# Performance work log

Hardware: AMD Instinct MI355X
Metric: run time of the kernel (lower is better)

Reference implementation:

```python
import math
import jax, jax.numpy as jnp
import numpy as np

N_ORDERS = 2
CHUNK = 64  # tokens per chunk (before virtual-token expansion)


def _expand_derivative(x, n):
    """expand_virtual_tokens(mode='derivative'): [B,H,S,D] -> [B,H,S*n,D]."""
    B, H, S, D = x.shape
    pad = jnp.zeros((B, H, n - 1, D), x.dtype)
    xp = jnp.concatenate([pad, x], axis=2)  # [B,H,S+n-1,D]
    coeffs = np.array([(-1) ** kk * math.comb(n - 1, kk) for kk in range(n)], dtype=np.float32)
    coeffs = coeffs / np.abs(coeffs).sum()  # L1-normalized binomial coeffs
    # window j at token t is x_pad[t+j]*coeffs[j]; then flip window dim (as in torch .flip(-1))
    win = jnp.stack([xp[:, :, j:j + S, :] * coeffs[j] for j in range(n)], axis=3)  # [B,H,S,n,D]
    win = win[:, :, :, ::-1, :]
    return win.reshape(B, H, S * n, D)


def _unlinear(x, scale=2.0):
    """unlinear_activation: gated norm-scaled gelu applied to inter-chunk state."""
    xn = jnp.linalg.norm(x, axis=-1, keepdims=True) + 1e-6
    return x / scale * jax.nn.gelu(scale * x / xn, approximate=True)


def _stab(x):
    # ensure_stability: clamp to [-1e4, 1e4], nan -> center (0)
    return jnp.nan_to_num(jnp.clip(x, -1e4, 1e4), nan=0.0, posinf=1e4, neginf=-1e4)


def _forward(q, k, v, beta):
    n = N_ORDERS
    B, H, S, D = q.shape
    qe = _expand_derivative(q, n)
    ke = _expand_derivative(k, n)
    ve = _expand_derivative(v, n)
    be = jnp.repeat(beta, n, axis=-1)[..., None]  # [B,H,S*n,1]
    w = ke * be  # delta-rule write keys
    u = ve * be  # delta-rule write values

    Cn = CHUNK * n                     # virtual tokens per chunk
    NC = (S * n) // Cn                 # number of chunks
    ch = lambda x: x.reshape(B, H, NC, Cn, D)
    qc, kc, wc, uc = ch(qe), ch(ke), ch(w), ch(u)

    # triangular (forward-substitution) inversion per chunk:
    # T = (I + tril(W K^T, -1))^{-1}  == fast_invert_matrix of the strictly-lower system
    A = jnp.tril(jnp.einsum('bhnid,bhnjd->bhnij', wc, kc), -1)
    eye = jnp.eye(Cn, dtype=q.dtype)
    T = jax.scipy.linalg.solve_triangular(
        eye + A, jnp.broadcast_to(eye, A.shape), lower=True, unit_diagonal=True)
    wci = jnp.einsum('bhnij,bhnjd->bhnid', T, wc)
    uci = jnp.einsum('bhnij,bhnjd->bhnid', T, uc)

    def chunk_step(h, xs):
        # sequential_delta_product_scan body: per-token Householder updates, n_orders steps
        qx, wx, ux = xs  # each [B,H,Cn,D]
        C = CHUNK
        qr = qx.reshape(B, H, C, n, D)
        wr = wx.reshape(B, H, C, n, D)
        ur = ux.reshape(B, H, C, n, D)
        state = jnp.broadcast_to(h[:, :, None], (B, H, C, D, D))  # per-token state
        outs = []
        for s in range(n):
            qs, ws, us = qr[:, :, :, s], wr[:, :, :, s], ur[:, :, :, s]
            kho = jnp.einsum('bhcd,bhcde->bhce', ws, state)
            uval = us - kho
            o_inter = jnp.einsum('bhcd,bhcde->bhce', qs, state)
            o_intra = qs * uval
            state = _stab(state + jnp.einsum('bhcd,bhce->bhcde', ws, uval))
            outs.append(o_intra + o_inter)
        o = jnp.stack(outs, axis=3).reshape(B, H, C * n, D)  # interleave: pos t*n+s
        h_new = _unlinear(state[:, :, -1])  # linear_activation=False path
        return h_new, o

    xs = (jnp.moveaxis(qc, 2, 0), jnp.moveaxis(wci, 2, 0), jnp.moveaxis(uci, 2, 0))
    h0 = jnp.zeros((B, H, D, D), q.dtype)
    _, os = jax.lax.scan(chunk_step, h0, xs)  # os: [NC,B,H,Cn,D]
    out_v = jnp.moveaxis(os, 0, 2).reshape(B, H, S, n, D)
    return out_v[..., n - 1, :]  # collapse virtual tokens: keep last-order output per token


def setup_inputs() -> dict:
    key = jax.random.key(0)
    kq, kk, kv, kb = jax.random.split(key, 4)
    B, H, S, D = 2, 16, 2048, 64
    return {
        'q': jax.random.normal(kq, (B, H, S, D), jnp.float32),
        'k': jax.random.normal(kk, (B, H, S, D), jnp.float32),
        'v': jax.random.normal(kv, (B, H, S, D), jnp.float32),
        'beta': jax.random.uniform(kb, (B, H, S), jnp.float32),
    }


def reference(q, k, v, beta):
    return _forward(q, k, v, beta)
```

## Files before the change

### kernel.cpp

```cpp
#include <hip/hip_runtime.h>
#include <math.h>


namespace {
constexpr int PAIRS = 32;
constexpr int SLEN  = 2048;
constexpr int D     = 64;
constexpr int CK    = 64;
constexpr int CN    = 128;
constexpr int NCH   = 32;
constexpr int NB2   = 16;
constexpr int NP    = 5;
constexpr size_t YWORDS = (size_t)PAIRS * NCH * CN * CN;
constexpr int GP = 2145;
constexpr size_t GGW = (size_t)PAIRS * NCH * GP;
constexpr size_t HGW = (size_t)PAIRS * (NCH + 1) * D * D;

__device__ __forceinline__ float stab1(float x) {
    float y = __builtin_amdgcn_fmed3f(x, -10000.f, 10000.f);
    return (x != x) ? 0.f : y;
}

__device__ __forceinline__ int kidx(int a, int f4) {
    return a * 68 + 4 * (f4 ^ ((a >> 2) & 3));
}
}

__global__ __launch_bounds__(256, 2)
void la_gram(const float* __restrict__ kg, float* __restrict__ gG)
{
    __shared__ float kstf[65 * 68];
    const int blk = blockIdx.x;
    const int p = blk >> 5, nc = blk & 31;
    const int tid = threadIdx.x;
    const int baseT = nc * CK;
    const float* kp = kg + (size_t)p * SLEN * D;

    for (int u = tid; u < 65 * 16; u += 256) {
        int a = u >> 4, f4 = u & 15;
        int src = baseT - 1 + a;
        float4 val = float4{0.f, 0.f, 0.f, 0.f};
        if (src >= 0) val = ((const float4*)(kp + (size_t)src * D))[f4];
        *(float4*)&kstf[kidx(a, f4)] = val;
    }
    __syncthreads();

    float* gps = gG + (size_t)blk * GP;
    for (int tt = tid; tt < 17 * 17; tt += 256) {
        int ta = tt / 17, tb = tt % 17;
        if (tb > ta) continue;
        int a0 = ta * 4, b0 = tb * 4;
        float acc[4][4] = {};
        for (int d4 = 0; d4 < 16; ++d4) {
            float4 av[4], bv[4];
            #pragma unroll
            for (int r = 0; r < 4; ++r) {
                av[r] = *(const float4*)&kstf[kidx(min(a0 + r, 64), d4)];
                bv[r] = *(const float4*)&kstf[kidx(min(b0 + r, 64), d4)];
            }
            #pragma unroll
            for (int r = 0; r < 4; ++r)
                #pragma unroll
                for (int c = 0; c < 4; ++c)
                    acc[r][c] += av[r].x * bv[c].x + av[r].y * bv[c].y
                               + av[r].z * bv[c].z + av[r].w * bv[c].w;
        }
        #pragma unroll
        for (int r = 0; r < 4; ++r)
            #pragma unroll
            for (int c = 0; c < 4; ++c) {
                int a = a0 + r, b = b0 + c;
                if (a <= 64 && b <= a)
                    gps[a * (a + 1) / 2 + b] = acc[r][c];
            }
    }
}

__global__ __launch_bounds__(256, 3)
void la_phase1g(const float* __restrict__ kg, const float* __restrict__ vg,
                const float* __restrict__ bg, float* __restrict__ ws,
                const float* __restrict__ gG)
{
    __shared__ float Ysh[CN][64];
    __shared__ float scm[2][CN][8];
    __shared__ float redsh[24][66];
    __shared__ float bq4[CK], bh[CK];

    const int blk  = blockIdx.x;
    const int p    = blk >> 6;
    const int nc   = (blk >> 1) & 31;
    const int half = blk & 1;
    const int tid  = threadIdx.x;
    const int col  = tid & 63;
    const int m    = tid >> 6;
    const int baseT = nc * CK;
    const float* kp = kg + (size_t)p * SLEN * D;
    const float* vp = vg + (size_t)p * SLEN * D;
    const float* bp = bg + (size_t)p * SLEN;
    const float* gps = gG + (size_t)(p * NCH + nc) * GP;

    if (tid < CK) {
        float bv = bp[baseT + tid];
        bq4[tid] = 0.25f * bv;
        bh[tid]  = 0.5f  * bv;
    }
    __syncthreads();

    const float* srcBase = half ? vp : kp;
    for (int u = tid; u < CN * 16; u += 256) {
        int i = u >> 4, f4 = u & 15;
        int ci = i >> 1, si = i & 1;
        float sc = si ? bh[ci] : -bh[ci];
        int srcT = baseT + ci - si;
        float4 val = float4{0.f, 0.f, 0.f, 0.f};
        if (srcT >= 0) val = ((const float4*)(srcBase + (size_t)srcT * D))[f4];
        val.x *= sc; val.y *= sc; val.z *= sc; val.w *= sc;
        *(float4*)&Ysh[i][f4 * 4] = val;
    }
    for (int e = tid; e < 64; e += 256) {
        int j = e >> 3, r = e & 7;
        int ai = (r >> 1) - (r & 1) + 1;
        int aj = (j >> 1) - (j & 1) + 1;
        int amax = max(ai, aj), amin = min(ai, aj);
        float sgn = ((r ^ j) & 1) ? -1.f : 1.f;
        scm[0][j][r] = sgn * bq4[r >> 1] * gps[amax * (amax + 1) / 2 + amin];
    }
    __syncthreads();

    for (int g = 0; g < 16; ++g) {
        const int buf = g & 1;
        float acc[8] = {};
        for (int j = m; j < 8 * g; j += 4) {
            float yv = Ysh[j][col];
            const float4 a03 = *(const float4*)&scm[buf][j][0];
            const float4 a47 = *(const float4*)&scm[buf][j][4];
            acc[0] += a03.x * yv; acc[1] += a03.y * yv;
            acc[2] += a03.z * yv; acc[3] += a03.w * yv;
            acc[4] += a47.x * yv; acc[5] += a47.y * yv;
            acc[6] += a47.z * yv; acc[7] += a47.w * yv;
        }
        if (m > 0) {
            #pragma unroll
            for (int r = 0; r < 8; ++r) redsh[(m - 1) * 8 + r][col] = acc[r];
        }
        __syncthreads();
        if (m == 0) {
            if (g > 0) {
                #pragma unroll
                for (int r = 0; r < 8; ++r)
                    acc[r] += redsh[r][col] + redsh[8 + r][col] + redsh[16 + r][col];
            }
            float yn[8];
            #pragma unroll
            for (int r = 0; r < 8; ++r) {
                float val = Ysh[8 * g + r][col] - acc[r];
                #pragma unroll
                for (int rp = 0; rp < 8; ++rp)
                    if (rp < r) val -= scm[buf][8 * g + rp][r] * yn[rp];
                yn[r] = val;
                Ysh[8 * g + r][col] = val;
            }
        } else if (g < 15) {
            const int T = g + 1, bufB = T & 1;
            const int nel = 8 * (8 * T + 8);
            for (int e = tid - 64; e < nel; e += 192) {
                int j = e >> 3, r = e & 7;
                int i = 8 * T + r;
                int ai = (i >> 1) - (i & 1) + 1;
                int aj = (j >> 1) - (j & 1) + 1;
                int amax = max(ai, aj), amin = min(ai, aj);
                float sgn = ((i ^ j) & 1) ? -1.f : 1.f;
                scm[bufB][j][r] = sgn * bq4[i >> 1] * gps[amax * (amax + 1) / 2 + amin];
            }
        }
        __syncthreads();
    }

    float* gY = ws + (size_t)(p * NCH + nc) * (CN * CN) + half * 64;
    for (int u = tid; u < CN * 16; u += 256) {
        int r = u >> 4, f4 = u & 15;
        *(float4*)&gY[r * CN + f4 * 4] = *(const float4*)&Ysh[r][f4 * 4];
    }
}

__global__ __launch_bounds__(512, 1)
void la_scan(const float* __restrict__ ws, float* __restrict__ hg)
{
    __shared__ float w0s[64], u0s[64], w1s[64], u1s[64];
    __shared__ float pA[8][64], pB[8][64];
    __shared__ float hsh2[64][67];

    const int p = blockIdx.x;
    const int tid = threadIdx.x;
    const int w = tid >> 6, lane = tid & 63;
    const int hd = tid >> 3, he0 = (tid & 7) * 8;
    const float* Yp = ws + (size_t)p * NCH * (CN * CN);
    float* hp = hg + (size_t)p * (NCH + 1) * (D * D);

    for (int idx = tid; idx < D * D; idx += 512) hp[idx] = 0.f;
    for (int idx = tid; idx < 64 * 67; idx += 512) (&hsh2[0][0])[idx] = 0.f;

    auto stagew = [&](float v) {
        if (tid < 64)       w0s[tid] = v;
        else if (tid < 128) u0s[tid - 64] = v;
        else if (tid < 192) w1s[tid - 128] = v;
        else if (tid < 256) u1s[tid - 192] = v;
    };
    {
        float v = 0.f;
        if (tid < 256) v = Yp[(size_t)(126 + (tid >> 7)) * CN + (tid & 127)];
        stagew(v);
    }
    float hs[8];
    #pragma unroll
    for (int j = 0; j < 8; ++j) hs[j] = 0.f;
    __syncthreads();

    for (int nc = 0; nc < NCH; ++nc) {
        float pf = 0.f;
        if (nc + 1 < NCH && tid < 256)
            pf = Yp[(size_t)(nc + 1) * (CN * CN)
                    + (size_t)(126 + (tid >> 7)) * CN + (tid & 127)];

        float s = 0.f;
        #pragma unroll
        for (int j = 0; j < 8; ++j) s += w0s[8 * w + j] * hs[j];
        pA[w][lane] = s;
        __syncthreads();

        float sum = 0.f;
        #pragma unroll
        for (int wv = 0; wv < 8; ++wv) sum += pA[wv][lane];
        const float uv0 = u0s[lane] - sum;

        float st1[8];
        float s2 = 0.f;
        #pragma unroll
        for (int j = 0; j < 8; ++j) {
            st1[j] = stab1(hs[j] + w0s[8 * w + j] * uv0);
            s2 += w1s[8 * w + j] * st1[j];
        }
        pB[w][lane] = s2;
        __syncthreads();

        float sum2 = 0.f;
        #pragma unroll
        for (int wv = 0; wv < 8; ++wv) sum2 += pB[wv][lane];
        const float uv1 = u1s[lane] - sum2;
        #pragma unroll
        for (int j = 0; j < 8; ++j)
            hsh2[8 * w + j][lane] = stab1(st1[j] + w1s[8 * w + j] * uv1);
        __syncthreads();

        {
            float st2v[8];
            float ssum = 0.f;
            #pragma unroll
            for (int j = 0; j < 8; ++j) {
                st2v[j] = hsh2[hd][he0 + j];
                ssum += st2v[j] * st2v[j];
            }
            ssum += __shfl_xor(ssum, 1);
            ssum += __shfl_xor(ssum, 2);
            ssum += __shfl_xor(ssum, 4);
            float xn = __builtin_amdgcn_sqrtf(ssum) + 1e-6f;
            float sc2 = 2.f * __builtin_amdgcn_rcpf(xn);
            float hn[8];
            #pragma unroll
            for (int j = 0; j < 8; ++j) {
                float x  = st2v[j];
                float y  = x * sc2;
                float y2 = y * y;
                float e  = __builtin_amdgcn_exp2f(y * (2.3022078f + 0.1029432f * y2));
                float th = (e - 1.f) * __builtin_amdgcn_rcpf(e + 1.f);
                hn[j] = 0.25f * x * y * (1.f + th);
                hsh2[hd][he0 + j] = hn[j];
            }
            float* ho = hp + (size_t)(nc + 1) * (D * D) + hd * 64 + he0;
            *(float4*)&ho[0] = float4{hn[0], hn[1], hn[2], hn[3]};
            *(float4*)&ho[4] = float4{hn[4], hn[5], hn[6], hn[7]};
        }
        if (nc + 1 < NCH) stagew(pf);
        __syncthreads();
        #pragma unroll
        for (int j = 0; j < 8; ++j) hs[j] = hsh2[8 * w + j][lane];
    }
}

__global__ __launch_bounds__(512)
void la_out(const float* __restrict__ qg, const float* __restrict__ ws,
            const float* __restrict__ hg, float* __restrict__ outg)
{
    __shared__ float hT[64 * 68];
    __shared__ float wbr[8][3][64];

    const int blk = blockIdx.x;
    const int p = blk >> 5, nc = blk & 31;
    const int tid = threadIdx.x;
    const int w = tid >> 6, lane = tid & 63;

    const float* Yc = ws + (size_t)(p * NCH + nc) * (CN * CN);
    const float* hp = hg + ((size_t)p * (NCH + 1) + nc) * (D * D);
    const float* qp = qg + (size_t)p * SLEN * D;
    float* op = outg + (size_t)p * SLEN * D;

    for (int idx = tid; idx < D * D; idx += 512) {
        int d = idx >> 6, e = idx & 63;
        hT[e * 68 + d] = hp[idx];
    }
    __syncthreads();

    float4 hr[16];
    #pragma unroll
    for (int k = 0; k < 16; ++k)
        hr[k] = *(const float4*)&hT[lane * 68 + 4 * k];

    for (int it = 0; it < 8; ++it) {
        const int c = it * 8 + w;
        const int t = nc * CK + c;
        const int srcT = (t > 0) ? t - 1 : 0;

        const float w0v = Yc[(size_t)(2 * c) * CN + lane];
        const float u0l = Yc[(size_t)(2 * c) * CN + 64 + lane];
        const float w1v = Yc[(size_t)(2 * c + 1) * CN + lane];
        const float u1l = Yc[(size_t)(2 * c + 1) * CN + 64 + lane];
        const float qv  = qp[(size_t)srcT * D + lane];
        wbr[w][0][lane] = w0v;
        wbr[w][1][lane] = w1v;
        wbr[w][2][lane] = qv;

        float uv0 = u0l;
        #pragma unroll
        for (int k = 0; k < 16; ++k) {
            float4 wb = *(const float4*)&wbr[w][0][4 * k];
            uv0 -= (wb.x * hr[k].x + wb.y * hr[k].y)
                 + (wb.z * hr[k].z + wb.w * hr[k].w);
        }
        float kh = 0.f, oa = 0.f;
        #pragma unroll
        for (int k = 0; k < 16; ++k) {
            float4 wb0 = *(const float4*)&wbr[w][0][4 * k];
            float4 wb1 = *(const float4*)&wbr[w][1][4 * k];
            float4 qb  = *(const float4*)&wbr[w][2][4 * k];
            float st0 = stab1(hr[k].x + wb0.x * uv0);
            float st1 = stab1(hr[k].y + wb0.y * uv0);
            float st2 = stab1(hr[k].z + wb0.z * uv0);
            float st3 = stab1(hr[k].w + wb0.w * uv0);
            kh += (wb1.x * st0 + wb1.y * st1) + (wb1.z * st2 + wb1.w * st3);
            oa += (qb.x * st0 + qb.y * st1) + (qb.z * st2 + qb.w * st3);
        }
        float uv1 = u1l - kh;
        float outv = 0.5f * (qv * uv1 + oa);
        op[(size_t)t * D + lane] = (t > 0) ? outv : 0.f;
    }
}

__global__ __launch_bounds__(256, 2)
void la_phase1f(const float* __restrict__ kg, const float* __restrict__ vg,
                const float* __restrict__ bg, float* __restrict__ ws)
{
    __shared__ float Ysh[CN][64];
    __shared__ float Gm[65][66];
    __shared__ char  ureg[17680];
    __shared__ float bq4[CK], bh[CK];

    float* kstf = (float*)ureg;
    float* scm  = (float*)ureg;
    float (*redsh)[66] = (float(*)[66])(ureg + 8192);

    const int blk  = blockIdx.x;
    const int p    = blk >> 6;
    const int nc   = (blk >> 1) & 31;
    const int half = blk & 1;
    const int tid  = threadIdx.x;
    const int baseT = nc * CK;
    const float* kp = kg + (size_t)p * SLEN * D;
    const float* vp = vg + (size_t)p * SLEN * D;
    const float* bp = bg + (size_t)p * SLEN;

    for (int u = tid; u < 65 * 16; u += 256) {
        int a = u >> 4, f4 = u & 15;
        int src = baseT - 1 + a;
        float4 val = float4{0.f, 0.f, 0.f, 0.f};
        if (src >= 0) val = ((const float4*)(kp + (size_t)src * D))[f4];
        *(float4*)&kstf[kidx(a, f4)] = val;
    }
    if (tid < CK) {
        float bv = bp[baseT + tid];
        bq4[tid] = 0.25f * bv;
        bh[tid]  = 0.5f  * bv;
    }
    __syncthreads();

    for (int u = tid; u < CN * 16; u += 256) {
        int i = u >> 4, f4 = u & 15;
        int ci = i >> 1, si = i & 1;
        float sc = si ? bh[ci] : -bh[ci];
        float4 val = float4{0.f, 0.f, 0.f, 0.f};
        if (half == 0) {
            val = *(const float4*)&kstf[kidx(ci - si + 1, f4)];
        } else {
            int srcT = baseT + ci - si;
            if (srcT >= 0) val = ((const float4*)(vp + (size_t)srcT * D))[f4];
        }
        val.x *= sc; val.y *= sc; val.z *= sc; val.w *= sc;
        *(float4*)&Ysh[i][f4 * 4] = val;
    }

    for (int tt = tid; tt < 17 * 17; tt += 256) {
        int ta = tt / 17, tb = tt % 17;
        if (tb > ta) continue;
        int a0 = ta * 4, b0 = tb * 4;
        float acc[4][4] = {};
        for (int d4 = 0; d4 < 16; ++d4) {
            float4 av[4], bv[4];
            #pragma unroll
            for (int r = 0; r < 4; ++r) {
                av[r] = *(const float4*)&kstf[kidx(min(a0 + r, 64), d4)];
                bv[r] = *(const float4*)&kstf[kidx(min(b0 + r, 64), d4)];
            }
            #pragma unroll
            for (int r = 0; r < 4; ++r)
                #pragma unroll
                for (int c = 0; c < 4; ++c)
                    acc[r][c] += av[r].x * bv[c].x + av[r].y * bv[c].y
                               + av[r].z * bv[c].z + av[r].w * bv[c].w;
        }
        #pragma unroll
        for (int r = 0; r < 4; ++r)
            #pragma unroll
            for (int c = 0; c < 4; ++c)
                if (a0 + r <= 64 && b0 + c <= 64) {
                    Gm[a0 + r][b0 + c] = acc[r][c];
                    Gm[b0 + c][a0 + r] = acc[r][c];
                }
    }
    __syncthreads();

    auto stripf = [&](int g, int t0, int tstride) {
        int buf = g & 1;
        int jmax = 8 * g + 8;
        for (int e = t0; e < 8 * jmax; e += tstride) {
            int j = e >> 3, r = e & 7;
            int i = 8 * g + r;
            int ai = (i >> 1) - (i & 1) + 1;
            int aj = (j >> 1) - (j & 1) + 1;
            float sgn = ((i ^ j) & 1) ? -1.f : 1.f;
            scm[(buf * CN + j) * 8 + r] = sgn * bq4[i >> 1] * Gm[ai][aj];
        }
    };

    stripf(0, tid, 256);
    __syncthreads();

    const int col = tid & 63;
    const int m   = tid >> 6;
    for (int g = 0; g < 16; ++g) {
        const int buf = g & 1;
        float acc[8] = {};
        for (int j = m; j < 8 * g; j += 4) {
            float yv = Ysh[j][col];
            const float4 a03 = *(const float4*)&scm[(buf * CN + j) * 8];
            const float4 a47 = *(const float4*)&scm[(buf * CN + j) * 8 + 4];
            acc[0] += a03.x * yv; acc[1] += a03.y * yv;
            acc[2] += a03.z * yv; acc[3] += a03.w * yv;
            acc[4] += a47.x * yv; acc[5] += a47.y * yv;
            acc[6] += a47.z * yv; acc[7] += a47.w * yv;
        }
        if (m > 0) {
            #pragma unroll
            for (int r = 0; r < 8; ++r) redsh[(m - 1) * 8 + r][col] = acc[r];
        }
        __syncthreads();
        if (m == 0) {
            if (g > 0) {
                #pragma unroll
                for (int r = 0; r < 8; ++r)
                    acc[r] += redsh[r][col] + redsh[8 + r][col] + redsh[16 + r][col];
            }
            float yn[8];
            #pragma unroll
            for (int r = 0; r < 8; ++r) {
                float val = Ysh[8 * g + r][col] - acc[r];
                #pragma unroll
                for (int rp = 0; rp < 8; ++rp)
                    if (rp < r) val -= scm[(buf * CN + 8 * g + rp) * 8 + r] * yn[rp];
                yn[r] = val;
                Ysh[8 * g + r][col] = val;
            }
        } else if (g < 15) {
            stripf(g + 1, tid - 64, 192);
        }
        __syncthreads();
    }

    float* gY = ws + (size_t)(p * NCH + nc) * (CN * CN) + half * 64;
    for (int u = tid; u < CN * 16; u += 256) {
        int r = u >> 4, f4 = u & 15;
        *(float4*)&gY[r * CN + f4 * 4] = *(const float4*)&Ysh[r][f4 * 4];
    }
}

__global__ __launch_bounds__(512, 4)
void la_phase2(const float* __restrict__ qg, const float* __restrict__ ws,
               float* __restrict__ outg)
{
    __shared__ float WU[2][NP][256];
    __shared__ float Qs[2][NP][64];
    __shared__ float pR1[8][NP][64];
    __shared__ float pKH[8][NP][64];
    __shared__ float pOA[8][NP][64];
    __shared__ float UV0[NP][64];
    __shared__ float UV1r[64];
    __shared__ float hsh[64][67];

    const int blk  = blockIdx.x;
    const int p    = blk >> 4, nb = blk & 15;
    const int tid  = threadIdx.x;
    const int w    = tid >> 6, lane = tid & 63;
    const int hd   = tid >> 3;
    const int he0  = (tid & 7) * 8;

    const float* qp = qg + (size_t)p * SLEN * D;
    float* op = outg + (size_t)p * SLEN * D;
    const float* wsbase = ws + (size_t)p * NCH * (CN * CN);

    const int cMain = nb * 4 + w;

    float4 wuR = float4{0.f, 0.f, 0.f, 0.f};
    float  qR  = 0.f;

    auto stage_load = [&](int nc) {
        const float* gY = wsbase + (size_t)nc * (CN * CN);
        if (w < 4) {
            wuR = *(const float4*)(gY + (size_t)(2 * cMain) * CN + lane * 4);
            int t = nc * CK + cMain;
            qR = qp[(size_t)((t > 0) ? t - 1 : 0) * D + lane];
        } else if (w == 4) {
            wuR = *(const float4*)(gY + (size_t)126 * CN + lane * 4);
            qR = qp[(size_t)(nc * CK + 62) * D + lane];
        }
    };
    auto stage_write = [&](int buf) {
        if (w < NP) {
            *(float4*)&WU[buf][w][lane * 4] = wuR;
            Qs[buf][w][lane] = qR;
        }
    };

    for (int idx = tid; idx < 64 * 67; idx += 512) (&hsh[0][0])[idx] = 0.f;
    stage_load(0);
    stage_write(0);
    __syncthreads();

    for (int nc = 0; nc < NCH; ++nc) {
        const int buf = nc & 1;
        float hs[8];
        #pragma unroll
        for (int j = 0; j < 8; ++j) hs[j] = hsh[8 * w + j][lane];
        if (nc + 1 < NCH) stage_load(nc + 1);

        #pragma unroll
        for (int P = 0; P < NP; ++P) {
            float4 a = *(const float4*)&WU[buf][P][8 * w];
            float4 b = *(const float4*)&WU[buf][P][8 * w + 4];
            pR1[w][P][lane] =
                  ((a.x * hs[0] + a.y * hs[1]) + (a.z * hs[2] + a.w * hs[3]))
                + ((b.x * hs[4] + b.y * hs[5]) + (b.z * hs[6] + b.w * hs[7]));
        }
        __syncthreads();

        if (w < NP) {
            float s = 0.f;
            #pragma unroll
            for (int wv = 0; wv < 8; ++wv) s += pR1[wv][w][lane];
            UV0[w][lane] = WU[buf][w][64 + lane] - s;
        }
        __syncthreads();

        #pragma unroll
        for (int P = 0; P < NP; ++P) {
            float uv0 = UV0[P][lane];
            float4 w0a = *(const float4*)&WU[buf][P][8 * w];
            float4 w0b = *(const float4*)&WU[buf][P][8 * w + 4];
            float4 w1a = *(const float4*)&WU[buf][P][128 + 8 * w];
            float4 w1b = *(const float4*)&WU[buf][P][128 + 8 * w + 4];
            float4 qa  = *(const float4*)&Qs[buf][P][8 * w];
            float4 qb  = *(const float4*)&Qs[buf][P][8 * w + 4];
            float st0 = stab1(hs[0] + w0a.x * uv0);
            float st1 = stab1(hs[1] + w0a.y * uv0);
            float st2 = stab1(hs[2] + w0a.z * uv0);
            float st3 = stab1(hs[3] + w0a.w * uv0);
            float st4 = stab1(hs[4] + w0b.x * uv0);
            float st5 = stab1(hs[5] + w0b.y * uv0);
            float st6 = stab1(hs[6] + w0b.z * uv0);
            float st7 = stab1(hs[7] + w0b.w * uv0);
            pKH[w][P][lane] =
                  ((w1a.x * st0 + w1a.y * st1) + (w1a.z * st2 + w1a.w * st3))
                + ((w1b.x * st4 + w1b.y * st5) + (w1b.z * st6 + w1b.w * st7));
            pOA[w][P][lane] =
                  ((qa.x * st0 + qa.y * st1) + (qa.z * st2 + qa.w * st3))
                + ((qb.x * st4 + qb.y * st5) + (qb.z * st6 + qb.w * st7));
        }
        stage_write(buf ^ 1);
        __syncthreads();

        if (w < 4) {
            float skh = 0.f, soa = 0.f;
            #pragma unroll
            for (int wv = 0; wv < 8; ++wv) {
                skh += pKH[wv][w][lane];
                soa += pOA[wv][w][lane];
            }
            float uv1 = WU[buf][w][192 + lane] - skh;
            int t = nc * CK + cMain;
            float outv = 0.5f * (Qs[buf][w][lane] * uv1 + soa);
            op[(size_t)t * D + lane] = (t > 0) ? outv : 0.f;
        } else if (w == 4) {
            float skh = 0.f;
            #pragma unroll
            for (int wv = 0; wv < 8; ++wv) skh += pKH[wv][4][lane];
            UV1r[lane] = WU[buf][4][192 + lane] - skh;
        }
        __syncthreads();

        {
            float w0d = WU[buf][4][hd];
            float w1d = WU[buf][4][128 + hd];
            float st2v[8];
            float ssum = 0.f;
            #pragma unroll
            for (int j = 0; j < 8; ++j) {
                float st1 = stab1(hsh[hd][he0 + j] + w0d * UV0[4][he0 + j]);
                float st2 = stab1(st1 + w1d * UV1r[he0 + j]);
                st2v[j] = st2;
                ssum += st2 * st2;
            }
            ssum += __shfl_xor(ssum, 1);
            ssum += __shfl_xor(ssum, 2);
            ssum += __shfl_xor(ssum, 4);
            float xn = __builtin_amdgcn_sqrtf(ssum) + 1e-6f;
            float s2 = 2.f * __builtin_amdgcn_rcpf(xn);
            #pragma unroll
            for (int j = 0; j < 8; ++j) {
                float x  = st2v[j];
                float y  = x * s2;
                float y2 = y * y;
                float e  = __builtin_amdgcn_exp2f(y * (2.3022078f + 0.1029432f * y2));
                float th = (e - 1.f) * __builtin_amdgcn_rcpf(e + 1.f);
                hsh[hd][he0 + j] = 0.25f * x * y * (1.f + th);
            }
        }
        __syncthreads();
    }
}

extern "C" void kernel_launch(void* const* d_in, const int* in_sizes, int n_in,
                              void* d_out, int out_size, void* d_ws, size_t ws_size,
                              hipStream_t stream)
{
    (void)in_sizes; (void)n_in; (void)out_size;
    const float* q    = (const float*)d_in[0];
    const float* k    = (const float*)d_in[1];
    const float* v    = (const float*)d_in[2];
    const float* beta = (const float*)d_in[3];
    float* ws  = (float*)d_ws;
    float* out = (float*)d_out;

    const size_t maxW  = (HGW > GGW) ? HGW : GGW;
    const size_t needA = (YWORDS + maxW) * sizeof(float);
    const size_t needB = (YWORDS + GGW) * sizeof(float);

    if (ws_size >= needA) {
        float* gG = ws + YWORDS;
        float* hg = ws + YWORDS;
        la_gram<<<PAIRS * NCH, 256, 0, stream>>>(k, gG);
        la_phase1g<<<PAIRS * NCH * 2, 256, 0, stream>>>(k, v, beta, ws, gG);
        la_scan<<<PAIRS, 512, 0, stream>>>(ws, hg);
        la_out<<<PAIRS * NCH, 512, 0, stream>>>(q, ws, hg, out);
    } else if (ws_size >= needB) {
        float* gG = ws + YWORDS;
        la_gram<<<PAIRS * NCH, 256, 0, stream>>>(k, gG);
        la_phase1g<<<PAIRS * NCH * 2, 256, 0, stream>>>(k, v, beta, ws, gG);
        la_phase2<<<PAIRS * NB2, 512, 0, stream>>>(q, ws, out);
    } else {
        la_phase1f<<<PAIRS * NCH * 2, 256, 0, stream>>>(k, v, beta, ws);
        la_phase2<<<PAIRS * NB2, 512, 0, stream>>>(q, ws, out);
    }
}
```

Measured before the change: 270.8 us.

## Unroll triangular solve inner loop, relax scan barriers, prefetch next token loads

```diff
diff --git a/kernel.cpp b/kernel.cpp
--- a/kernel.cpp
+++ b/kernel.cpp
@@ -24,6 +24,10 @@
 __device__ __forceinline__ int kidx(int a, int f4) {
     return a * 68 + 4 * (f4 ^ ((a >> 2) & 3));
 }
+
+__device__ __forceinline__ void bar_lds() {
+    asm volatile("s_waitcnt lgkmcnt(0)\n\ts_barrier" ::: "memory");
+}
 }
 
 __global__ __launch_bounds__(256, 2)
@@ -129,15 +133,41 @@
 
     for (int g = 0; g < 16; ++g) {
         const int buf = g & 1;
+        const int jmax = 8 * g;
         float acc[8] = {};
-        for (int j = m; j < 8 * g; j += 4) {
-            float yv = Ysh[j][col];
-            const float4 a03 = *(const float4*)&scm[buf][j][0];
-            const float4 a47 = *(const float4*)&scm[buf][j][4];
-            acc[0] += a03.x * yv; acc[1] += a03.y * yv;
-            acc[2] += a03.z * yv; acc[3] += a03.w * yv;
-            acc[4] += a47.x * yv; acc[5] += a47.y * yv;
-            acc[6] += a47.z * yv; acc[7] += a47.w * yv;
+        {
+            int j = m;
+            for (; j + 12 < jmax; j += 16) {
+                float y0 = Ysh[j][col];
+                float y1 = Ysh[j + 4][col];
+                float y2 = Ysh[j + 8][col];
+                float y3 = Ysh[j + 12][col];
+                const float4 a0 = *(const float4*)&scm[buf][j][0];
+                const float4 b0 = *(const float4*)&scm[buf][j][4];
+                const float4 a1 = *(const float4*)&scm[buf][j + 4][0];
+                const float4 b1 = *(const float4*)&scm[buf][j + 4][4];
+                const float4 a2 = *(const float4*)&scm[buf][j + 8][0];
+                const float4 b2 = *(const float4*)&scm[buf][j + 8][4];
+                const float4 a3 = *(const float4*)&scm[buf][j + 12][0];
+                const float4 b3 = *(const float4*)&scm[buf][j + 12][4];
+                acc[0] += a0.x * y0 + a1.x * y1 + a2.x * y2 + a3.x * y3;
+                acc[1] += a0.y * y0 + a1.y * y1 + a2.y * y2 + a3.y * y3;
+                acc[2] += a0.z * y0 + a1.z * y1 + a2.z * y2 + a3.z * y3;
+                acc[3] += a0.w * y0 + a1.w * y1 + a2.w * y2 + a3.w * y3;
+                acc[4] += b0.x * y0 + b1.x * y1 + b2.x * y2 + b3.x * y3;
+                acc[5] += b0.y * y0 + b1.y * y1 + b2.y * y2 + b3.y * y3;
+                acc[6] += b0.z * y0 + b1.z * y1 + b2.z * y2 + b3.z * y3;
+                acc[7] += b0.w * y0 + b1.w * y1 + b2.w * y2 + b3.w * y3;
+            }
+            for (; j < jmax; j += 4) {
+                float yv = Ysh[j][col];
+                const float4 a03 = *(const float4*)&scm[buf][j][0];
+                const float4 a47 = *(const float4*)&scm[buf][j][4];
+                acc[0] += a03.x * yv; acc[1] += a03.y * yv;
+                acc[2] += a03.z * yv; acc[3] += a03.w * yv;
+                acc[4] += a47.x * yv; acc[5] += a47.y * yv;
+                acc[6] += a47.z * yv; acc[7] += a47.w * yv;
+            }
         }
         if (m > 0) {
             #pragma unroll
@@ -226,7 +256,7 @@
         #pragma unroll
         for (int j = 0; j < 8; ++j) s += w0s[8 * w + j] * hs[j];
         pA[w][lane] = s;
-        __syncthreads();
+        bar_lds();
 
         float sum = 0.f;
         #pragma unroll
@@ -241,7 +271,7 @@
             s2 += w1s[8 * w + j] * st1[j];
         }
         pB[w][lane] = s2;
-        __syncthreads();
+        bar_lds();
 
         float sum2 = 0.f;
         #pragma unroll
@@ -250,7 +280,7 @@
         #pragma unroll
         for (int j = 0; j < 8; ++j)
             hsh2[8 * w + j][lane] = stab1(st1[j] + w1s[8 * w + j] * uv1);
-        __syncthreads();
+        bar_lds();
 
         {
             float st2v[8];
@@ -281,7 +311,7 @@
             *(float4*)&ho[4] = float4{hn[4], hn[5], hn[6], hn[7]};
         }
         if (nc + 1 < NCH) stagew(pf);
-        __syncthreads();
+        bar_lds();
         #pragma unroll
         for (int j = 0; j < 8; ++j) hs[j] = hsh2[8 * w + j][lane];
     }
@@ -315,16 +345,29 @@
     for (int k = 0; k < 16; ++k)
         hr[k] = *(const float4*)&hT[lane * 68 + 4 * k];
 
+    float w0n, u0n, w1n, u1n, qn;
+    {
+        const int c = w, t = nc * CK + c;
+        w0n = Yc[(size_t)(2 * c) * CN + lane];
+        u0n = Yc[(size_t)(2 * c) * CN + 64 + lane];
+        w1n = Yc[(size_t)(2 * c + 1) * CN + lane];
+        u1n = Yc[(size_t)(2 * c + 1) * CN + 64 + lane];
+        qn  = qp[(size_t)((t > 0) ? t - 1 : 0) * D + lane];
+    }
+
     for (int it = 0; it < 8; ++it) {
         const int c = it * 8 + w;
         const int t = nc * CK + c;
-        const int srcT = (t > 0) ? t - 1 : 0;
-
-        const float w0v = Yc[(size_t)(2 * c) * CN + lane];
-        const float u0l = Yc[(size_t)(2 * c) * CN + 64 + lane];
-        const float w1v = Yc[(size_t)(2 * c + 1) * CN + lane];
-        const float u1l = Yc[(size_t)(2 * c + 1) * CN + 64 + lane];
-        const float qv  = qp[(size_t)srcT * D + lane];
+        const float w0v = w0n, u0l = u0n, w1v = w1n, u1l = u1n, qv = qn;
+        if (it < 7) {
+            const int c2 = (it + 1) * 8 + w;
+            w0n = Yc[(size_t)(2 * c2) * CN + lane];
+            u0n = Yc[(size_t)(2 * c2) * CN + 64 + lane];
+            w1n = Yc[(size_t)(2 * c2 + 1) * CN + lane];
+            u1n = Yc[(size_t)(2 * c2 + 1) * CN + 64 + lane];
+            qn  = qp[(size_t)(nc * CK + c2 - 1) * D + lane];
+        }
+
         wbr[w][0][lane] = w0v;
         wbr[w][1][lane] = w1v;
         wbr[w][2][lane] = qv;
```

Measured after the change: 266.4 us. About the same (-1.6%).
